# Kernel optimization log

Measured on AMD Instinct MI355X. Metric: run time of the kernel, lower is better.

The kernel has to match this reference:

```python
import jax, jax.numpy as jnp
from jax import lax
import numpy as np

I, H = 2048, 128
EPS = 1e-5


def setup_inputs() -> dict:
    key = jax.random.key(0)
    ks = jax.random.split(key, 12)
    s_ih = 1.0 / np.sqrt(H)  # torch nn.RNN init: U(-1/sqrt(H), 1/sqrt(H))
    s_fc = 1.0 / np.sqrt(H)
    u = lambda k, shape, s: jax.random.uniform(k, shape, jnp.float32, -s, s)
    return {
        "x": jax.random.normal(ks[0], (64, 512, I), jnp.float32),
        "W_ih": u(ks[1], (H, I), s_ih),
        "b_ih": u(ks[2], (H,), s_ih),
        "W_hh": u(ks[3], (H, H), s_ih),
        "b_hh": u(ks[4], (H,), s_ih),
        "W1": u(ks[5], (H, H), s_fc),
        "b1": u(ks[6], (H,), s_fc),
        "W2": u(ks[7], (H, H), s_fc),
        "b2": u(ks[8], (H,), s_fc),
        "gamma": jnp.ones((H,), jnp.float32),
        "beta": jnp.zeros((H,), jnp.float32),
    }


def reference(x, W_ih, b_ih, W_hh, b_hh, W1, b1, W2, b2, gamma, beta):
    B = x.shape[0]
    # Precompute input projection for all timesteps: [B, T, H]
    xp = jnp.einsum('bti,hi->bth', x, W_ih) + b_ih

    def step(h, xt):  # h: [B, H], xt: [B, H]
        h_new = jnp.tanh(xt + h @ W_hh.T + b_hh)
        return h_new, None

    h0 = jnp.zeros((B, H), x.dtype)
    hT, _ = lax.scan(step, h0, jnp.swapaxes(xp, 0, 1))  # scan over T

    z = jax.nn.relu(hT @ W1.T + b1)
    z = jax.nn.relu(z @ W2.T + b2)
    mu = jnp.mean(z, axis=-1, keepdims=True)
    var = jnp.mean(jnp.square(z - mu), axis=-1, keepdims=True)
    return gamma * (z - mu) * lax.rsqrt(var + EPS) + beta
```

## Files before the change

### kernel.cpp

```cpp
#include <hip/hip_runtime.h>


typedef __bf16 bf16x8 __attribute__((ext_vector_type(8)));
typedef float  f32x4  __attribute__((ext_vector_type(4)));

#define T_STEPS 512
#define I_DIM   2048
#define H_DIM   128
#define B_DIM   64
#define M_TOT   (B_DIM * T_STEPS)

#define LDS_BARRIER() asm volatile("s_waitcnt lgkmcnt(0)\n\ts_barrier" ::: "memory")

__device__ __forceinline__ unsigned short f2bf(float f) {
    unsigned int u = __float_as_uint(f);
    u += 0x7FFFu + ((u >> 16) & 1u);
    return (unsigned short)(u >> 16);
}
__device__ __forceinline__ float bf2f(unsigned short u) {
    return __uint_as_float(((unsigned int)u) << 16);
}
__device__ __forceinline__ bf16x8 packbf8(float4 lo, float4 hi) {
    union { bf16x8 v; unsigned short u[8]; } r;
    r.u[0] = f2bf(lo.x); r.u[1] = f2bf(lo.y); r.u[2] = f2bf(lo.z); r.u[3] = f2bf(lo.w);
    r.u[4] = f2bf(hi.x); r.u[5] = f2bf(hi.y); r.u[6] = f2bf(hi.z); r.u[7] = f2bf(hi.w);
    return r.v;
}
__device__ __forceinline__ float tanh5(float a) {
    float m = a * 2.88539008f;
    float q = __builtin_amdgcn_exp2f(m);
    float r = __builtin_amdgcn_rcpf(q + 1.f);
    return __builtin_fmaf(-2.f, r, 1.f);
}
__device__ __forceinline__ unsigned int pack2bf(float a, float b) {
    unsigned int ua = __float_as_uint(a) + 0x8000u;
    unsigned int ub = __float_as_uint(b) + 0x8000u;
    return __builtin_amdgcn_perm(ub, ua, 0x07060302u);
}

#define BM  64
#define BK  64
#define LDK 72
#define NKT (I_DIM / BK)

__global__ __launch_bounds__(256) void gemm_xp(
    const float* __restrict__ x, const float* __restrict__ w,
    const float* __restrict__ b_ih, const float* __restrict__ b_hh,
    float* __restrict__ xp)
{
    __shared__ __align__(16) unsigned short As[BM * LDK];
    __shared__ __align__(16) unsigned short Bs[H_DIM * LDK];

    const int tid = threadIdx.x;
    const int m0  = blockIdx.x * BM;
    const int r0  = tid >> 4;
    const int c4  = tid & 15;
    const int lane = tid & 63, wave = tid >> 6;
    const int wm = (wave >> 1) * 32;
    const int wn = (wave & 1) * 64;
    const int l16 = lane & 15, quad = lane >> 4;

    f32x4 acc[2][4] = {};
    float4 ar[2][4], br[2][8];

    auto load_tiles = [&](int s, int k0) {
        #pragma unroll
        for (int i = 0; i < 4; ++i)
            ar[s][i] = *(const float4*)(x + (size_t)(m0 + i * 16 + r0) * I_DIM + k0 + c4 * 4);
        #pragma unroll
        for (int i = 0; i < 8; ++i)
            br[s][i] = *(const float4*)(w + (size_t)(i * 16 + r0) * I_DIM + k0 + c4 * 4);
    };
    auto store_tiles = [&](int s) {
        #pragma unroll
        for (int i = 0; i < 4; ++i) {
            ushort4 v; v.x = f2bf(ar[s][i].x); v.y = f2bf(ar[s][i].y);
                       v.z = f2bf(ar[s][i].z); v.w = f2bf(ar[s][i].w);
            *(ushort4*)(As + (i * 16 + r0) * LDK + c4 * 4) = v;
        }
        #pragma unroll
        for (int i = 0; i < 8; ++i) {
            ushort4 v; v.x = f2bf(br[s][i].x); v.y = f2bf(br[s][i].y);
                       v.z = f2bf(br[s][i].z); v.w = f2bf(br[s][i].w);
            *(ushort4*)(Bs + (i * 16 + r0) * LDK + c4 * 4) = v;
        }
    };
    auto mfma_tile = [&]() {
        #pragma unroll
        for (int kt = 0; kt < 2; ++kt) {
            bf16x8 af[2], bfr[4];
            #pragma unroll
            for (int i = 0; i < 2; ++i)
                af[i] = *(const bf16x8*)(As + (wm + i * 16 + l16) * LDK + kt * 32 + quad * 8);
            #pragma unroll
            for (int j = 0; j < 4; ++j)
                bfr[j] = *(const bf16x8*)(Bs + (wn + j * 16 + l16) * LDK + kt * 32 + quad * 8);
            #pragma unroll
            for (int i = 0; i < 2; ++i)
                #pragma unroll
                for (int j = 0; j < 4; ++j)
                    acc[i][j] = __builtin_amdgcn_mfma_f32_16x16x32_bf16(af[i], bfr[j], acc[i][j], 0, 0, 0);
        }
    };

    load_tiles(0, 0);
    load_tiles(1, BK);

    for (int ii = 0; ii < NKT / 2; ++ii) {
        #pragma unroll
        for (int s = 0; s < 2; ++s) {
            const int i  = ii * 2 + s;
            LDS_BARRIER();
            store_tiles(s);
            const int kn = (i + 2) * BK;
            if (kn < I_DIM) load_tiles(s, kn);
            LDS_BARRIER();
            mfma_tile();
        }
    }

    #pragma unroll
    for (int j = 0; j < 4; ++j) {
        const int col = wn + j * 16 + l16;
        const float bias = b_ih[col] + b_hh[col];
        #pragma unroll
        for (int i = 0; i < 2; ++i)
            #pragma unroll
            for (int r = 0; r < 4; ++r) {
                const int row = wm + i * 16 + quad * 4 + r;
                xp[(size_t)(m0 + row) * H_DIM + col] = acc[i][j][r] + bias;
            }
    }
}

#define NB  16
#define LDH 136

__global__ __launch_bounds__(256) void rnn_scan(
    const float* __restrict__ xp,
    const float* __restrict__ Whh,
    const float* __restrict__ W1, const float* __restrict__ b1,
    const float* __restrict__ W2, const float* __restrict__ b2,
    const float* __restrict__ gamma, const float* __restrict__ beta,
    float* __restrict__ out)
{
    __shared__ __align__(16) unsigned short hbuf[2][NB * LDH];
    __shared__ float ztmp[NB][129];
    __shared__ float ztmp2[NB][129];

    const int tid  = threadIdx.x;
    const int lane = tid & 63, w = tid >> 6;
    const int l16  = lane & 15, quad = lane >> 4;
    const int b0   = blockIdx.x * NB;

    bf16x8 afr[2][4];
    #pragma unroll
    for (int t = 0; t < 2; ++t) {
        const float* wrow = Whh + (32 * w + 16 * t + l16) * H_DIM;
        #pragma unroll
        for (int ks = 0; ks < 4; ++ks) {
            float4 lo = *(const float4*)(wrow + 32 * ks + 8 * quad);
            float4 hi = *(const float4*)(wrow + 32 * ks + 8 * quad + 4);
            afr[t][ks] = packbf8(lo, hi);
        }
    }

    const float* xpb = xp + (size_t)(b0 + l16) * T_STEPS * H_DIM + 32 * w + 4 * quad;

    float4 xr0[4], xr1[4];
    #pragma unroll
    for (int d = 0; d < 4; ++d) {
        xr0[d] = *(const float4*)(xpb + (size_t)d * H_DIM);
        xr1[d] = *(const float4*)(xpb + (size_t)d * H_DIM + 16);
    }

    for (int i = tid; i < NB * LDH; i += 256) hbuf[0][i] = 0;
    __syncthreads();

    const int rbase = l16 * LDH + quad * 8;
    const int wbase = l16 * LDH + 32 * w + 4 * quad;

    for (int t = 0; t < T_STEPS; t += 4) {
        #pragma unroll
        for (int u = 0; u < 4; ++u) {
            const int tt = t + u;
            const unsigned short* hb = hbuf[tt & 1];
            bf16x8 bf0 = *(const bf16x8*)(hb + rbase);
            bf16x8 bf1 = *(const bf16x8*)(hb + rbase + 32);
            bf16x8 bf2 = *(const bf16x8*)(hb + rbase + 64);
            bf16x8 bf3 = *(const bf16x8*)(hb + rbase + 96);

            f32x4 c0 = {xr0[u].x, xr0[u].y, xr0[u].z, xr0[u].w};
            f32x4 c1 = {xr1[u].x, xr1[u].y, xr1[u].z, xr1[u].w};
            int tn = tt + 4; if (tn > T_STEPS - 1) tn = T_STEPS - 1;
            xr0[u] = *(const float4*)(xpb + (size_t)tn * H_DIM);
            xr1[u] = *(const float4*)(xpb + (size_t)tn * H_DIM + 16);

            f32x4 p0 = __builtin_amdgcn_mfma_f32_16x16x32_bf16(afr[0][0], bf0, c0, 0, 0, 0);
            f32x4 p1 = __builtin_amdgcn_mfma_f32_16x16x32_bf16(afr[1][0], bf0, c1, 0, 0, 0);
            p0 = __builtin_amdgcn_mfma_f32_16x16x32_bf16(afr[0][1], bf1, p0, 0, 0, 0);
            p1 = __builtin_amdgcn_mfma_f32_16x16x32_bf16(afr[1][1], bf1, p1, 0, 0, 0);
            p0 = __builtin_amdgcn_mfma_f32_16x16x32_bf16(afr[0][2], bf2, p0, 0, 0, 0);
            p1 = __builtin_amdgcn_mfma_f32_16x16x32_bf16(afr[1][2], bf2, p1, 0, 0, 0);
            p0 = __builtin_amdgcn_mfma_f32_16x16x32_bf16(afr[0][3], bf3, p0, 0, 0, 0);
            p1 = __builtin_amdgcn_mfma_f32_16x16x32_bf16(afr[1][3], bf3, p1, 0, 0, 0);

            unsigned short* hn = hbuf[(tt + 1) & 1];
            unsigned int w00 = pack2bf(tanh5(p0[0]), tanh5(p0[1]));
            unsigned int w01 = pack2bf(tanh5(p0[2]), tanh5(p0[3]));
            *(uint2*)(hn + wbase) = make_uint2(w00, w01);
            unsigned int w10 = pack2bf(tanh5(p1[0]), tanh5(p1[1]));
            unsigned int w11 = pack2bf(tanh5(p1[2]), tanh5(p1[3]));
            *(uint2*)(hn + wbase + 16) = make_uint2(w10, w11);

            LDS_BARRIER();
        }
    }

    const int n  = tid >> 4;
    const int j0 = (tid & 15) * 8;
    const unsigned short* hT = hbuf[0] + n * LDH;

    float s[8];
    #pragma unroll
    for (int i = 0; i < 8; ++i) s[i] = b1[j0 + i];
    for (int k = 0; k < H_DIM; ++k) {
        float hv = bf2f(hT[k]);
        #pragma unroll
        for (int i = 0; i < 8; ++i) s[i] += hv * W1[(j0 + i) * H_DIM + k];
    }
    #pragma unroll
    for (int i = 0; i < 8; ++i) ztmp[n][j0 + i] = fmaxf(s[i], 0.f);
    __syncthreads();

    #pragma unroll
    for (int i = 0; i < 8; ++i) s[i] = b2[j0 + i];
    for (int k = 0; k < H_DIM; ++k) {
        float zv = ztmp[n][k];
        #pragma unroll
        for (int i = 0; i < 8; ++i) s[i] += zv * W2[(j0 + i) * H_DIM + k];
    }
    #pragma unroll
    for (int i = 0; i < 8; ++i) ztmp2[n][j0 + i] = fmaxf(s[i], 0.f);
    __syncthreads();

    float sum = 0.f, sq = 0.f;
    #pragma unroll
    for (int i = 0; i < 8; ++i) { float v = ztmp2[n][j0 + i]; sum += v; sq += v * v; }
    #pragma unroll
    for (int o = 1; o < 16; o <<= 1) { sum += __shfl_xor(sum, o); sq += __shfl_xor(sq, o); }
    float mu   = sum * (1.f / 128.f);
    float var  = sq * (1.f / 128.f) - mu * mu;
    float rstd = rsqrtf(var + 1e-5f);
    #pragma unroll
    for (int i = 0; i < 8; ++i) {
        int j = j0 + i;
        out[(size_t)(b0 + n) * H_DIM + j] =
            gamma[j] * (ztmp2[n][j] - mu) * rstd + beta[j];
    }
}

extern "C" void kernel_launch(void* const* d_in, const int* in_sizes, int n_in,
                              void* d_out, int out_size, void* d_ws, size_t ws_size,
                              hipStream_t stream) {
    const float* x     = (const float*)d_in[0];
    const float* W_ih  = (const float*)d_in[1];
    const float* b_ih  = (const float*)d_in[2];
    const float* W_hh  = (const float*)d_in[3];
    const float* b_hh  = (const float*)d_in[4];
    const float* W1    = (const float*)d_in[5];
    const float* b1    = (const float*)d_in[6];
    const float* W2    = (const float*)d_in[7];
    const float* b2    = (const float*)d_in[8];
    const float* gamma = (const float*)d_in[9];
    const float* beta  = (const float*)d_in[10];
    float* out = (float*)d_out;

    float* xp = (float*)d_ws;

    gemm_xp<<<dim3(M_TOT / BM), dim3(256), 0, stream>>>(x, W_ih, b_ih, b_hh, xp);
    rnn_scan<<<dim3(B_DIM / NB), dim3(256), 0, stream>>>(xp, W_hh, W1, b1, W2, b2,
                                                         gamma, beta, out);
}
```

Measured before the change: 671.8 us.

## Run RNN scan in a single wavefront per block to remove barriers

The recurrent scan now runs with one 64-lane wavefront per 16-sequence block. Each wave holds all of W_hh in registers and does all 8 output tiles itself, so the per-timestep LDS barrier across four waves goes away and the exchange happens within one wave through LDS. The tanh scale constant is folded into W_hh and into the xp projection epilogue, which removes a multiply per element in the serial loop. The FC layers and layernorm move to MFMA in bf16, which loses some precision. Each step now does four times the MFMA work on a single wave, so fewer SIMDs are used per block.

```diff
diff --git a/kernel.cpp b/kernel.cpp
--- a/kernel.cpp
+++ b/kernel.cpp
@@ -9,6 +9,7 @@
 #define H_DIM   128
 #define B_DIM   64
 #define M_TOT   (B_DIM * T_STEPS)
+#define KTANH   2.88539008f
 
 #define LDS_BARRIER() asm volatile("s_waitcnt lgkmcnt(0)\n\ts_barrier" ::: "memory")
 
@@ -17,18 +18,16 @@
     u += 0x7FFFu + ((u >> 16) & 1u);
     return (unsigned short)(u >> 16);
 }
-__device__ __forceinline__ float bf2f(unsigned short u) {
-    return __uint_as_float(((unsigned int)u) << 16);
-}
-__device__ __forceinline__ bf16x8 packbf8(float4 lo, float4 hi) {
+__device__ __forceinline__ bf16x8 packbf8(float4 lo, float4 hi, float scale) {
     union { bf16x8 v; unsigned short u[8]; } r;
-    r.u[0] = f2bf(lo.x); r.u[1] = f2bf(lo.y); r.u[2] = f2bf(lo.z); r.u[3] = f2bf(lo.w);
-    r.u[4] = f2bf(hi.x); r.u[5] = f2bf(hi.y); r.u[6] = f2bf(hi.z); r.u[7] = f2bf(hi.w);
+    r.u[0] = f2bf(lo.x * scale); r.u[1] = f2bf(lo.y * scale);
+    r.u[2] = f2bf(lo.z * scale); r.u[3] = f2bf(lo.w * scale);
+    r.u[4] = f2bf(hi.x * scale); r.u[5] = f2bf(hi.y * scale);
+    r.u[6] = f2bf(hi.z * scale); r.u[7] = f2bf(hi.w * scale);
     return r.v;
 }
-__device__ __forceinline__ float tanh5(float a) {
-    float m = a * 2.88539008f;
-    float q = __builtin_amdgcn_exp2f(m);
+__device__ __forceinline__ float tanhp(float x) {
+    float q = __builtin_amdgcn_exp2f(x);
     float r = __builtin_amdgcn_rcpf(q + 1.f);
     return __builtin_fmaf(-2.f, r, 1.f);
 }
@@ -122,21 +121,20 @@
     #pragma unroll
     for (int j = 0; j < 4; ++j) {
         const int col = wn + j * 16 + l16;
-        const float bias = b_ih[col] + b_hh[col];
+        const float biask = (b_ih[col] + b_hh[col]) * KTANH;
         #pragma unroll
         for (int i = 0; i < 2; ++i)
             #pragma unroll
             for (int r = 0; r < 4; ++r) {
                 const int row = wm + i * 16 + quad * 4 + r;
-                xp[(size_t)(m0 + row) * H_DIM + col] = acc[i][j][r] + bias;
+                xp[(size_t)(m0 + row) * H_DIM + col] = fmaf(acc[i][j][r], KTANH, biask);
             }
     }
 }
 
-#define NB  16
-#define LDH 136
-
-__global__ __launch_bounds__(256) void rnn_scan(
+#define NBW 16
+
+__global__ __launch_bounds__(64) void rnn_scan(
     const float* __restrict__ xp,
     const float* __restrict__ Whh,
     const float* __restrict__ W1, const float* __restrict__ b1,
@@ -144,119 +142,154 @@
     const float* __restrict__ gamma, const float* __restrict__ beta,
     float* __restrict__ out)
 {
-    __shared__ __align__(16) unsigned short hbuf[2][NB * LDH];
-    __shared__ float ztmp[NB][129];
-    __shared__ float ztmp2[NB][129];
-
-    const int tid  = threadIdx.x;
-    const int lane = tid & 63, w = tid >> 6;
-    const int l16  = lane & 15, quad = lane >> 4;
-    const int b0   = blockIdx.x * NB;
-
-    bf16x8 afr[2][4];
-    #pragma unroll
-    for (int t = 0; t < 2; ++t) {
-        const float* wrow = Whh + (32 * w + 16 * t + l16) * H_DIM;
+    __shared__ __align__(16) unsigned int hl[16 * 64];
+
+    const int lane = threadIdx.x;
+    const int n = lane & 15, q = lane >> 4;
+    const int b0 = blockIdx.x * NBW;
+
+    bf16x8 aW[8][4];
+    #pragma unroll
+    for (int i = 0; i < 8; ++i) {
+        const float* wrow = Whh + (16 * i + n) * H_DIM;
         #pragma unroll
         for (int ks = 0; ks < 4; ++ks) {
-            float4 lo = *(const float4*)(wrow + 32 * ks + 8 * quad);
-            float4 hi = *(const float4*)(wrow + 32 * ks + 8 * quad + 4);
-            afr[t][ks] = packbf8(lo, hi);
-        }
-    }
-
-    const float* xpb = xp + (size_t)(b0 + l16) * T_STEPS * H_DIM + 32 * w + 4 * quad;
-
-    float4 xr0[4], xr1[4];
-    #pragma unroll
-    for (int d = 0; d < 4; ++d) {
-        xr0[d] = *(const float4*)(xpb + (size_t)d * H_DIM);
-        xr1[d] = *(const float4*)(xpb + (size_t)d * H_DIM + 16);
-    }
-
-    for (int i = tid; i < NB * LDH; i += 256) hbuf[0][i] = 0;
-    __syncthreads();
-
-    const int rbase = l16 * LDH + quad * 8;
-    const int wbase = l16 * LDH + 32 * w + 4 * quad;
-
-    for (int t = 0; t < T_STEPS; t += 4) {
-        #pragma unroll
-        for (int u = 0; u < 4; ++u) {
-            const int tt = t + u;
-            const unsigned short* hb = hbuf[tt & 1];
-            bf16x8 bf0 = *(const bf16x8*)(hb + rbase);
-            bf16x8 bf1 = *(const bf16x8*)(hb + rbase + 32);
-            bf16x8 bf2 = *(const bf16x8*)(hb + rbase + 64);
-            bf16x8 bf3 = *(const bf16x8*)(hb + rbase + 96);
-
-            f32x4 c0 = {xr0[u].x, xr0[u].y, xr0[u].z, xr0[u].w};
-            f32x4 c1 = {xr1[u].x, xr1[u].y, xr1[u].z, xr1[u].w};
-            int tn = tt + 4; if (tn > T_STEPS - 1) tn = T_STEPS - 1;
-            xr0[u] = *(const float4*)(xpb + (size_t)tn * H_DIM);
-            xr1[u] = *(const float4*)(xpb + (size_t)tn * H_DIM + 16);
-
-            f32x4 p0 = __builtin_amdgcn_mfma_f32_16x16x32_bf16(afr[0][0], bf0, c0, 0, 0, 0);
-            f32x4 p1 = __builtin_amdgcn_mfma_f32_16x16x32_bf16(afr[1][0], bf0, c1, 0, 0, 0);
-            p0 = __builtin_amdgcn_mfma_f32_16x16x32_bf16(afr[0][1], bf1, p0, 0, 0, 0);
-            p1 = __builtin_amdgcn_mfma_f32_16x16x32_bf16(afr[1][1], bf1, p1, 0, 0, 0);
-            p0 = __builtin_amdgcn_mfma_f32_16x16x32_bf16(afr[0][2], bf2, p0, 0, 0, 0);
-            p1 = __builtin_amdgcn_mfma_f32_16x16x32_bf16(afr[1][2], bf2, p1, 0, 0, 0);
-            p0 = __builtin_amdgcn_mfma_f32_16x16x32_bf16(afr[0][3], bf3, p0, 0, 0, 0);
-            p1 = __builtin_amdgcn_mfma_f32_16x16x32_bf16(afr[1][3], bf3, p1, 0, 0, 0);
-
-            unsigned short* hn = hbuf[(tt + 1) & 1];
-            unsigned int w00 = pack2bf(tanh5(p0[0]), tanh5(p0[1]));
-            unsigned int w01 = pack2bf(tanh5(p0[2]), tanh5(p0[3]));
-            *(uint2*)(hn + wbase) = make_uint2(w00, w01);
-            unsigned int w10 = pack2bf(tanh5(p1[0]), tanh5(p1[1]));
-            unsigned int w11 = pack2bf(tanh5(p1[2]), tanh5(p1[3]));
-            *(uint2*)(hn + wbase + 16) = make_uint2(w10, w11);
-
-            LDS_BARRIER();
-        }
-    }
-
-    const int n  = tid >> 4;
-    const int j0 = (tid & 15) * 8;
-    const unsigned short* hT = hbuf[0] + n * LDH;
-
-    float s[8];
-    #pragma unroll
-    for (int i = 0; i < 8; ++i) s[i] = b1[j0 + i];
-    for (int k = 0; k < H_DIM; ++k) {
-        float hv = bf2f(hT[k]);
-        #pragma unroll
-        for (int i = 0; i < 8; ++i) s[i] += hv * W1[(j0 + i) * H_DIM + k];
-    }
-    #pragma unroll
-    for (int i = 0; i < 8; ++i) ztmp[n][j0 + i] = fmaxf(s[i], 0.f);
-    __syncthreads();
-
-    #pragma unroll
-    for (int i = 0; i < 8; ++i) s[i] = b2[j0 + i];
-    for (int k = 0; k < H_DIM; ++k) {
-        float zv = ztmp[n][k];
-        #pragma unroll
-        for (int i = 0; i < 8; ++i) s[i] += zv * W2[(j0 + i) * H_DIM + k];
-    }
-    #pragma unroll
-    for (int i = 0; i < 8; ++i) ztmp2[n][j0 + i] = fmaxf(s[i], 0.f);
-    __syncthreads();
-
-    float sum = 0.f, sq = 0.f;
-    #pragma unroll
-    for (int i = 0; i < 8; ++i) { float v = ztmp2[n][j0 + i]; sum += v; sq += v * v; }
-    #pragma unroll
-    for (int o = 1; o < 16; o <<= 1) { sum += __shfl_xor(sum, o); sq += __shfl_xor(sq, o); }
-    float mu   = sum * (1.f / 128.f);
+            float4 lo = *(const float4*)(wrow + 32 * ks + 8 * q);
+            float4 hi = *(const float4*)(wrow + 32 * ks + 8 * q + 4);
+            aW[i][ks] = packbf8(lo, hi, KTANH);
+        }
+    }
+
+    const float* xpb = xp + (size_t)(b0 + n) * T_STEPS * H_DIM + 4 * q;
+
+    f32x4 cin[2][8];
+    #pragma unroll
+    for (int s = 0; s < 2; ++s)
+        #pragma unroll
+        for (int i = 0; i < 8; ++i)
+            cin[s][i] = *(const f32x4*)(xpb + (size_t)s * H_DIM + 16 * i);
+
+    union { uint4 u; bf16x8 v; } hz; hz.u = make_uint4(0, 0, 0, 0);
+    bf16x8 hb[4];
+    #pragma unroll
+    for (int ks = 0; ks < 4; ++ks) hb[ks] = hz.v;
+
+    const int wb0 = n * 4 + 2 * (q & 1) + (q >> 1) * 64;
+    const int rb0 = q * 64 + n * 4;
+
+    for (int t = 0; t < T_STEPS; ++t) {
+        const int s = t & 1;
+        f32x4 acc[8];
+        #pragma unroll
+        for (int i = 0; i < 8; ++i)
+            acc[i] = __builtin_amdgcn_mfma_f32_16x16x32_bf16(aW[i][0], hb[0], cin[s][i], 0, 0, 0);
+        {
+            int tn = t + 2; if (tn > T_STEPS - 1) tn = T_STEPS - 1;
+            #pragma unroll
+            for (int i = 0; i < 8; ++i)
+                cin[s][i] = *(const f32x4*)(xpb + (size_t)tn * H_DIM + 16 * i);
+        }
+        #pragma unroll
+        for (int ks = 1; ks < 4; ++ks)
+            #pragma unroll
+            for (int i = 0; i < 8; ++i)
+                acc[i] = __builtin_amdgcn_mfma_f32_16x16x32_bf16(aW[i][ks], hb[ks], acc[i], 0, 0, 0);
+        #pragma unroll
+        for (int i = 0; i < 8; ++i) {
+            uint2 pk;
+            pk.x = pack2bf(tanhp(acc[i][0]), tanhp(acc[i][1]));
+            pk.y = pack2bf(tanhp(acc[i][2]), tanhp(acc[i][3]));
+            *(uint2*)(hl + wb0 + 2 * i * 64) = pk;
+        }
+        #pragma unroll
+        for (int ks = 0; ks < 4; ++ks)
+            hb[ks] = *(const bf16x8*)(hl + rb0 + ks * 256);
+    }
+
+    bf16x8 wf[8][4];
+    #pragma unroll
+    for (int i = 0; i < 8; ++i) {
+        const float* wrow = W1 + (16 * i + n) * H_DIM;
+        #pragma unroll
+        for (int ks = 0; ks < 4; ++ks) {
+            float4 lo = *(const float4*)(wrow + 32 * ks + 8 * q);
+            float4 hi = *(const float4*)(wrow + 32 * ks + 8 * q + 4);
+            wf[i][ks] = packbf8(lo, hi, 1.f);
+        }
+    }
+    {
+        f32x4 z[8];
+        #pragma unroll
+        for (int i = 0; i < 8; ++i) {
+            float4 bv = *(const float4*)(b1 + 16 * i + 4 * q);
+            f32x4 c = {bv.x, bv.y, bv.z, bv.w};
+            z[i] = __builtin_amdgcn_mfma_f32_16x16x32_bf16(wf[i][0], hb[0], c, 0, 0, 0);
+        }
+        #pragma unroll
+        for (int ks = 1; ks < 4; ++ks)
+            #pragma unroll
+            for (int i = 0; i < 8; ++i)
+                z[i] = __builtin_amdgcn_mfma_f32_16x16x32_bf16(wf[i][ks], hb[ks], z[i], 0, 0, 0);
+        #pragma unroll
+        for (int i = 0; i < 8; ++i) {
+            uint2 pk;
+            pk.x = pack2bf(fmaxf(z[i][0], 0.f), fmaxf(z[i][1], 0.f));
+            pk.y = pack2bf(fmaxf(z[i][2], 0.f), fmaxf(z[i][3], 0.f));
+            *(uint2*)(hl + wb0 + 2 * i * 64) = pk;
+        }
+        #pragma unroll
+        for (int ks = 0; ks < 4; ++ks)
+            hb[ks] = *(const bf16x8*)(hl + rb0 + ks * 256);
+    }
+
+    #pragma unroll
+    for (int i = 0; i < 8; ++i) {
+        const float* wrow = W2 + (16 * i + n) * H_DIM;
+        #pragma unroll
+        for (int ks = 0; ks < 4; ++ks) {
+            float4 lo = *(const float4*)(wrow + 32 * ks + 8 * q);
+            float4 hi = *(const float4*)(wrow + 32 * ks + 8 * q + 4);
+            wf[i][ks] = packbf8(lo, hi, 1.f);
+        }
+    }
+    f32x4 z2[8];
+    #pragma unroll
+    for (int i = 0; i < 8; ++i) {
+        float4 bv = *(const float4*)(b2 + 16 * i + 4 * q);
+        f32x4 c = {bv.x, bv.y, bv.z, bv.w};
+        z2[i] = __builtin_amdgcn_mfma_f32_16x16x32_bf16(wf[i][0], hb[0], c, 0, 0, 0);
+    }
+    #pragma unroll
+    for (int ks = 1; ks < 4; ++ks)
+        #pragma unroll
+        for (int i = 0; i < 8; ++i)
+            z2[i] = __builtin_amdgcn_mfma_f32_16x16x32_bf16(wf[i][ks], hb[ks], z2[i], 0, 0, 0);
+
+    float sm = 0.f, sq = 0.f;
+    #pragma unroll
+    for (int i = 0; i < 8; ++i)
+        #pragma unroll
+        for (int r = 0; r < 4; ++r) {
+            float v = fmaxf(z2[i][r], 0.f);
+            z2[i][r] = v;
+            sm += v; sq += v * v;
+        }
+    sm += __shfl_xor(sm, 16); sq += __shfl_xor(sq, 16);
+    sm += __shfl_xor(sm, 32); sq += __shfl_xor(sq, 32);
+    float mu   = sm * (1.f / 128.f);
     float var  = sq * (1.f / 128.f) - mu * mu;
     float rstd = rsqrtf(var + 1e-5f);
-    #pragma unroll
-    for (int i = 0; i < 8; ++i) {
-        int j = j0 + i;
-        out[(size_t)(b0 + n) * H_DIM + j] =
-            gamma[j] * (ztmp2[n][j] - mu) * rstd + beta[j];
+    float* op = out + (size_t)(b0 + n) * H_DIM + 4 * q;
+    #pragma unroll
+    for (int i = 0; i < 8; ++i) {
+        float4 g  = *(const float4*)(gamma + 16 * i + 4 * q);
+        float4 bt = *(const float4*)(beta  + 16 * i + 4 * q);
+        float4 o;
+        o.x = fmaf(g.x * rstd, z2[i][0] - mu, bt.x);
+        o.y = fmaf(g.y * rstd, z2[i][1] - mu, bt.y);
+        o.z = fmaf(g.z * rstd, z2[i][2] - mu, bt.z);
+        o.w = fmaf(g.w * rstd, z2[i][3] - mu, bt.w);
+        *(float4*)(op + 16 * i) = o;
     }
 }
 
@@ -279,6 +312,6 @@
     float* xp = (float*)d_ws;
 
     gemm_xp<<<dim3(M_TOT / BM), dim3(256), 0, stream>>>(x, W_ih, b_ih, b_hh, xp);
-    rnn_scan<<<dim3(B_DIM / NB), dim3(256), 0, stream>>>(xp, W_hh, W1, b1, W2, b2,
+    rnn_scan<<<dim3(B_DIM / NBW), dim3(64), 0, stream>>>(xp, W_hh, W1, b1, W2, b2,
                                                          gamma, beta, out);
 }
```

After: 1.141 ms. 69.9% more time.
